# Kernel tuning notes

Measured on AMD Instinct MI355X. Metric: run time of the kernel, lower is better.

Reference implementation:

```python
import jax, jax.numpy as jnp
import numpy as np
from jax import lax

DIM = 128
TOPW = 4
SCALE = DIM ** (-0.5)


def setup_inputs() -> dict:
    key = jax.random.key(0)
    kq, ki = jax.random.split(key)
    query = jax.random.normal(kq, (4, 4096, DIM), dtype=jnp.float32)
    image = jax.random.normal(ki, (4, 8192, DIM), dtype=jnp.float32)
    return {"query": query, "image": image}


def reference(query, image):
    # diff_routing=False: inputs are detached in torch; no effect on fwd values.
    # attn: (b, Nq, mn) = scaled QK^T
    attn = jnp.einsum('bqc,bmc->bqm', query, image) * SCALE
    _, topw_index = lax.top_k(attn, TOPW)  # (b, Nq, topw)
    return topw_index
```

## Files before the change

kernel.cpp:

```cpp
#include <hip/hip_runtime.h>
#include <float.h>
#include <stdint.h>


#define NBATCH 4
#define NQ 4096
#define NM 8192
#define KD 128

typedef unsigned short ushort_t;
typedef __attribute__((ext_vector_type(8))) short bf16x8;
typedef __attribute__((ext_vector_type(16))) float f32x16;

#define BETTER64(v, i, w, j) (((v) > (w)) || ((v) == (w) && (i) < (j)))

__device__ inline float fmed3(float a, float b, float c) {
#if __has_builtin(__builtin_amdgcn_fmed3f)
  return __builtin_amdgcn_fmed3f(a, b, c);
#else
  return fmaxf(fminf(a, b), fminf(fmaxf(a, b), c));
#endif
}

__device__ inline ushort_t f2bf(float f) {
  unsigned u = __float_as_uint(f);
  u += 0x7fffu + ((u >> 16) & 1u);
  return (ushort_t)(u >> 16);
}

__global__ __launch_bounds__(256) void wr_cvt(const float* __restrict__ qry,
                                              const float* __restrict__ img,
                                              ushort_t* __restrict__ qb,
                                              int4* __restrict__ ib) {
  const int blk = (int)blockIdx.x;
  const int tid = (int)threadIdx.x;
  if (blk < 2048) {
    const int t = blk * 256 + tid;
    const float4 v = ((const float4*)qry)[t];
    ushort4 o;
    o.x = f2bf(v.x); o.y = f2bf(v.y); o.z = f2bf(v.z); o.w = f2bf(v.w);
    ((ushort4*)qb)[t] = o;
  } else {
    const int tg = blk - 2048;
    const int b = tg >> 8;
    const int tile = tg & 255;
    __shared__ __align__(16) ushort_t T[32 * 128];
    {
      const int r = tid >> 3;
      const int seg = tid & 7;
      const float* src = img + ((size_t)(b * NM + tile * 32 + r)) * KD + seg * 16;
      ushort_t tmp[16];
#pragma unroll
      for (int i = 0; i < 4; ++i) {
        const float4 v = ((const float4*)src)[i];
        tmp[i * 4 + 0] = f2bf(v.x);
        tmp[i * 4 + 1] = f2bf(v.y);
        tmp[i * 4 + 2] = f2bf(v.z);
        tmp[i * 4 + 3] = f2bf(v.w);
      }
      const int c0 = (seg * 16 + r * 8) & 127;
      const int c1 = (seg * 16 + 8 + r * 8) & 127;
      *(int4*)&T[r * 128 + c0] = *(const int4*)&tmp[0];
      *(int4*)&T[r * 128 + c1] = *(const int4*)&tmp[8];
    }
    __syncthreads();
    int4* dstt = ib + ((size_t)b * 256 + tile) * 512;
#pragma unroll
    for (int h = 0; h < 2; ++h) {
      const int n = tid + h * 256;
      const int c = n >> 6;
      const int l = n & 63;
      const int ml = l & 31;
      const int col = (c * 16 + (l >> 5) * 8 + ml * 8) & 127;
      dstt[n] = *(const int4*)&T[ml * 128 + col];
    }
  }
}

__global__ __launch_bounds__(512, 2) void wr_mfma(const float* __restrict__ qry,
                                                  const float* __restrict__ img,
                                                  const ushort_t* __restrict__ qb,
                                                  const int4* __restrict__ ib,
                                                  int* __restrict__ out) {
  const int bid = (int)blockIdx.x;
  const int b = (bid & 7) >> 1;
  const int qt = ((bid >> 3) << 1) | (bid & 1);
  const int qbase = qt * 32;

  const int tid = (int)threadIdx.x;
  const int lane = tid & 63;
  const int w = tid >> 6;
  const int qc = lane & 31;
  const int kh = lane >> 5;

  const ushort_t* Qb = qb + ((size_t)b * NQ + qbase) * KD;
  const int4* ibc = ib + (size_t)b * 131072;

  bf16x8 bfrag[8];
  {
    const ushort_t* p = Qb + (size_t)qc * KD + kh * 8;
#pragma unroll
    for (int c = 0; c < 8; ++c) bfrag[c] = *(const bf16x8*)(p + c * 16);
  }

  float tva[4], tvb[4];
#pragma unroll
  for (int s = 0; s < 4; ++s) { tva[s] = -FLT_MAX; tvb[s] = -FLT_MAX; }

  bf16x8 bufA[8], bufB[8];

  auto loadTile = [&](bf16x8* buf, int T) {
    const int4* p = ibc + ((((w * 32 + T) << 9)) + lane);
#pragma unroll
    for (int c = 0; c < 8; ++c) buf[c] = *(const bf16x8*)(p + c * 64);
  };

  auto compute = [&](const bf16x8* buf, int vb) {
    f32x16 acc;
#pragma unroll
    for (int r = 0; r < 16; ++r) acc[r] = 0.0f;
#pragma unroll
    for (int c = 0; c < 8; ++c)
      acc = __builtin_amdgcn_mfma_f32_32x32x16_bf16(buf[c], bfrag[c], acc, 0, 0, 0);
#pragma unroll
    for (int r = 0; r < 16; ++r) {
      const int rc = (r & 3) + 8 * (r >> 2);
      const unsigned kb =
          (__float_as_uint(acc[r]) & 0xFFFFF800u) | (unsigned)(vb - rc);
      const float key = __uint_as_float(kb);
      if (r & 1) {
        tvb[3] = fmed3(key, tvb[2], tvb[3]);
        tvb[2] = fmed3(key, tvb[1], tvb[2]);
        tvb[1] = fmed3(key, tvb[0], tvb[1]);
        tvb[0] = fmaxf(tvb[0], key);
      } else {
        tva[3] = fmed3(key, tva[2], tva[3]);
        tva[2] = fmed3(key, tva[1], tva[2]);
        tva[1] = fmed3(key, tva[0], tva[1]);
        tva[0] = fmaxf(tva[0], key);
      }
    }
  };

  int vb = 2047 - 4 * kh;
  loadTile(bufA, 0);
  loadTile(bufB, 1);
  for (int T = 0; T < 32; T += 2) {
    compute(bufA, vb);
    if (T + 2 < 32) loadTile(bufA, T + 2);
    compute(bufB, vb - 32);
    if (T + 3 < 32) loadTile(bufB, T + 3);
    vb -= 64;
  }

#pragma unroll
  for (int e = 0; e < 4; ++e) {
    const float key = tvb[e];
    tva[3] = fmed3(key, tva[2], tva[3]);
    tva[2] = fmed3(key, tva[1], tva[2]);
    tva[1] = fmed3(key, tva[0], tva[1]);
    tva[0] = fmaxf(tva[0], key);
  }

  {
    float keys[4];
#pragma unroll
    for (int e = 0; e < 4; ++e) keys[e] = __shfl_down(tva[e], 32, 64);
#pragma unroll
    for (int e = 0; e < 4; ++e) {
      const float key = keys[e];
      tva[3] = fmed3(key, tva[2], tva[3]);
      tva[2] = fmed3(key, tva[1], tva[2]);
      tva[1] = fmed3(key, tva[0], tva[1]);
      tva[0] = fmaxf(tva[0], key);
    }
  }

  __shared__ float ck[32][33];
  __shared__ int top8[32][8];
  __shared__ double pd[32][8];
  __shared__ int pi[32][8];

  if (kh == 0) {
#pragma unroll
    for (int s = 0; s < 4; ++s) ck[qc][w * 4 + s] = tva[s];
  }
  __syncthreads();

  for (int p = tid; p < 1024; p += 512) {
    const int q = p >> 5;
    const int j = p & 31;
    const float k = ck[q][j];
    int rank = 0;
#pragma unroll 8
    for (int i = 0; i < 32; ++i) {
      const float o = ck[q][i];
      rank += (o > k) || (o == k && i < j);
    }
    if (rank < 8) {
      const unsigned bits = __float_as_uint(k);
      top8[q][rank] = (j >> 2) * 1024 + 2047 - (int)(bits & 0x7FFu);
    }
  }
  __syncthreads();

  if (tid < 256) {
    const int q = tid >> 3;
    const int slot = tid & 7;
    const int m = top8[q][slot];
    const float* qrow = qry + ((size_t)b * NQ + qbase + q) * KD;
    const float* irow = img + ((size_t)b * NM + m) * KD;
    double s0 = 0.0, s1 = 0.0, s2 = 0.0, s3 = 0.0;
#pragma unroll
    for (int k = 0; k < KD; k += 4) {
      const float4 xv = *(const float4*)(qrow + k);
      const float4 yv = *(const float4*)(irow + k);
      s0 = fma((double)xv.x, (double)yv.x, s0);
      s1 = fma((double)xv.y, (double)yv.y, s1);
      s2 = fma((double)xv.z, (double)yv.z, s2);
      s3 = fma((double)xv.w, (double)yv.w, s3);
    }
    pd[q][slot] = (s0 + s1) + (s2 + s3);
    pi[q][slot] = m;
  }
  __syncthreads();

  if (tid < 32) {
    const int q = tid;
    double fv[4];
    int fi[4];
#pragma unroll
    for (int e = 0; e < 4; ++e) { fv[e] = -DBL_MAX; fi[e] = 0x7fffffff; }
    for (int sl = 0; sl < 8; ++sl) {
      const double v = pd[q][sl];
      const int m = pi[q][sl];
      const bool b0 = BETTER64(v, m, fv[0], fi[0]);
      const bool b1 = BETTER64(v, m, fv[1], fi[1]);
      const bool b2 = BETTER64(v, m, fv[2], fi[2]);
      const bool b3 = BETTER64(v, m, fv[3], fi[3]);
      fv[3] = b2 ? fv[2] : (b3 ? v : fv[3]);
      fi[3] = b2 ? fi[2] : (b3 ? m : fi[3]);
      fv[2] = b1 ? fv[1] : (b2 ? v : fv[2]);
      fi[2] = b1 ? fi[1] : (b2 ? m : fi[2]);
      fv[1] = b0 ? fv[0] : (b1 ? v : fv[1]);
      fi[1] = b0 ? fi[0] : (b1 ? m : fi[1]);
      fv[0] = b0 ? v : fv[0];
      fi[0] = b0 ? m : fi[0];
    }
    int4 o;
    o.x = fi[0]; o.y = fi[1]; o.z = fi[2]; o.w = fi[3];
    *(int4*)(out + ((size_t)b * NQ + qbase + q) * 4) = o;
  }
}

#define QT 64
#define MT 128
#define KC 64
#define NTHREADS 512

__global__ __launch_bounds__(NTHREADS) void wr_main(const float* __restrict__ qry,
                                                    const float* __restrict__ img,
                                                    int* __restrict__ out) {
  __shared__ __align__(16) float A_lds[KD * QT];
  __shared__ __align__(16) float B_lds[KC * MT];

  const int t = (int)threadIdx.x;
  const int b = (int)blockIdx.x >> 6;
  const int qbase = ((int)blockIdx.x & 63) * QT;

  const float* qp = qry + ((size_t)b * NQ + qbase) * KD;
  const float* ip = img + (size_t)b * NM * KD;

  {
    const int r = t >> 3;
    const int kc = t & 7;
    const float* src = qp + (size_t)r * KD;
#pragma unroll
    for (int i = 0; i < 4; ++i) {
      const int k0 = kc * 4 + i * 32;
      const float4 v = *(const float4*)(src + k0);
      A_lds[(k0 + 0) * QT + r] = v.x;
      A_lds[(k0 + 1) * QT + r] = v.y;
      A_lds[(k0 + 2) * QT + r] = v.z;
      A_lds[(k0 + 3) * QT + r] = v.w;
    }
  }

  const int qi = t >> 5;
  const int mi = t & 31;

  float tv[4][4];
  int ti[4][4];
#pragma unroll
  for (int j = 0; j < 4; ++j)
#pragma unroll
    for (int s = 0; s < 4; ++s) { tv[j][s] = -FLT_MAX; ti[j][s] = 0x7fffffff; }

  for (int tile = 0; tile < NM / MT; ++tile) {
    const int mbase = tile * MT;
    float acc[4][4];
#pragma unroll
    for (int j = 0; j < 4; ++j)
#pragma unroll
      for (int s = 0; s < 4; ++s) acc[j][s] = 0.0f;

    for (int kb = 0; kb < KD; kb += KC) {
      __syncthreads();
      {
        const int r = t >> 2;
        const int kc = t & 3;
        const float* src = ip + (size_t)(mbase + r) * KD + kb;
#pragma unroll
        for (int i = 0; i < 4; ++i) {
          const int k0 = kc * 4 + i * 16;
          const float4 v = *(const float4*)(src + k0);
          B_lds[(k0 + 0) * MT + r] = v.x;
          B_lds[(k0 + 1) * MT + r] = v.y;
          B_lds[(k0 + 2) * MT + r] = v.z;
          B_lds[(k0 + 3) * MT + r] = v.w;
        }
      }
      __syncthreads();

#pragma unroll 8
      for (int k = 0; k < KC; ++k) {
        const float4 av = *(const float4*)&A_lds[(kb + k) * QT + qi * 4];
        const float4 bv = *(const float4*)&B_lds[k * MT + mi * 4];
        acc[0][0] = fmaf(av.x, bv.x, acc[0][0]);
        acc[0][1] = fmaf(av.x, bv.y, acc[0][1]);
        acc[0][2] = fmaf(av.x, bv.z, acc[0][2]);
        acc[0][3] = fmaf(av.x, bv.w, acc[0][3]);
        acc[1][0] = fmaf(av.y, bv.x, acc[1][0]);
        acc[1][1] = fmaf(av.y, bv.y, acc[1][1]);
        acc[1][2] = fmaf(av.y, bv.z, acc[1][2]);
        acc[1][3] = fmaf(av.y, bv.w, acc[1][3]);
        acc[2][0] = fmaf(av.z, bv.x, acc[2][0]);
        acc[2][1] = fmaf(av.z, bv.y, acc[2][1]);
        acc[2][2] = fmaf(av.z, bv.z, acc[2][2]);
        acc[2][3] = fmaf(av.z, bv.w, acc[2][3]);
        acc[3][0] = fmaf(av.w, bv.x, acc[3][0]);
        acc[3][1] = fmaf(av.w, bv.y, acc[3][1]);
        acc[3][2] = fmaf(av.w, bv.z, acc[3][2]);
        acc[3][3] = fmaf(av.w, bv.w, acc[3][3]);
      }
    }

#pragma unroll
    for (int j = 0; j < 4; ++j) {
#pragma unroll
      for (int s = 0; s < 4; ++s) {
        const float v = acc[j][s];
        const int m = mbase + mi * 4 + s;
        const bool b0 = v > tv[j][0];
        const bool b1 = v > tv[j][1];
        const bool b2 = v > tv[j][2];
        const bool b3 = v > tv[j][3];
        tv[j][3] = b2 ? tv[j][2] : (b3 ? v : tv[j][3]);
        ti[j][3] = b2 ? ti[j][2] : (b3 ? m : ti[j][3]);
        tv[j][2] = b1 ? tv[j][1] : (b2 ? v : tv[j][2]);
        ti[j][2] = b1 ? ti[j][1] : (b2 ? m : ti[j][2]);
        tv[j][1] = b0 ? tv[j][0] : (b1 ? v : tv[j][1]);
        ti[j][1] = b0 ? ti[j][0] : (b1 ? m : ti[j][1]);
        tv[j][0] = b0 ? v : tv[j][0];
        ti[j][0] = b0 ? m : ti[j][0];
      }
    }
  }

  __syncthreads();
  int* idx_lds = (int*)B_lds;
#pragma unroll
  for (int j = 0; j < 4; ++j)
#pragma unroll
    for (int s = 0; s < 4; ++s)
      idx_lds[(qi * 4 + j) * 128 + mi * 4 + s] = ti[j][s];
  __syncthreads();

  double* pv = (double*)A_lds;
  int* piL = (int*)(A_lds + 4096);
  {
    const int r = t >> 3;
    const int slot = t & 7;
    const float* qrow = qp + (size_t)r * KD;
    double bv[4];
    int bi[4];
#pragma unroll
    for (int e = 0; e < 4; ++e) { bv[e] = -DBL_MAX; bi[e] = 0x7fffffff; }

    for (int c = 0; c < 16; ++c) {
      const int m = idx_lds[r * 128 + slot * 16 + c];
      const float* irow = ip + (size_t)m * KD;
      double s0 = 0.0, s1 = 0.0, s2 = 0.0, s3 = 0.0;
#pragma unroll
      for (int k = 0; k < KD; k += 4) {
        const float4 xv = *(const float4*)(qrow + k);
        const float4 yv = *(const float4*)(irow + k);
        s0 = fma((double)xv.x, (double)yv.x, s0);
        s1 = fma((double)xv.y, (double)yv.y, s1);
        s2 = fma((double)xv.z, (double)yv.z, s2);
        s3 = fma((double)xv.w, (double)yv.w, s3);
      }
      const double v = (s0 + s1) + (s2 + s3);
      const bool b0 = BETTER64(v, m, bv[0], bi[0]);
      const bool b1 = BETTER64(v, m, bv[1], bi[1]);
      const bool b2 = BETTER64(v, m, bv[2], bi[2]);
      const bool b3 = BETTER64(v, m, bv[3], bi[3]);
      bv[3] = b2 ? bv[2] : (b3 ? v : bv[3]);
      bi[3] = b2 ? bi[2] : (b3 ? m : bi[3]);
      bv[2] = b1 ? bv[1] : (b2 ? v : bv[2]);
      bi[2] = b1 ? bi[1] : (b2 ? m : bi[2]);
      bv[1] = b0 ? bv[0] : (b1 ? v : bv[1]);
      bi[1] = b0 ? bi[0] : (b1 ? m : bi[1]);
      bv[0] = b0 ? v : bv[0];
      bi[0] = b0 ? m : bi[0];
    }
#pragma unroll
    for (int e = 0; e < 4; ++e) {
      pv[t * 4 + e] = bv[e];
      piL[t * 4 + e] = bi[e];
    }
  }
  __syncthreads();

  if (t < QT) {
    double fv[4];
    int fi[4];
#pragma unroll
    for (int e = 0; e < 4; ++e) { fv[e] = -DBL_MAX; fi[e] = 0x7fffffff; }
    for (int sl = 0; sl < 8; ++sl) {
#pragma unroll
      for (int e = 0; e < 4; ++e) {
        const double v = pv[(t * 8 + sl) * 4 + e];
        const int m = piL[(t * 8 + sl) * 4 + e];
        const bool b0 = BETTER64(v, m, fv[0], fi[0]);
        const bool b1 = BETTER64(v, m, fv[1], fi[1]);
        const bool b2 = BETTER64(v, m, fv[2], fi[2]);
        const bool b3 = BETTER64(v, m, fv[3], fi[3]);
        fv[3] = b2 ? fv[2] : (b3 ? v : fv[3]);
        fi[3] = b2 ? fi[2] : (b3 ? m : fi[3]);
        fv[2] = b1 ? fv[1] : (b2 ? v : fv[2]);
        fi[2] = b1 ? fi[1] : (b2 ? m : fi[2]);
        fv[1] = b0 ? fv[0] : (b1 ? v : fv[1]);
        fi[1] = b0 ? fi[0] : (b1 ? m : fi[1]);
        fv[0] = b0 ? v : fv[0];
        fi[0] = b0 ? m : fi[0];
      }
    }
    int4 o;
    o.x = fi[0]; o.y = fi[1]; o.z = fi[2]; o.w = fi[3];
    *(int4*)(out + ((size_t)b * NQ + qbase + t) * 4) = o;
  }
}

extern "C" void kernel_launch(void* const* d_in, const int* in_sizes, int n_in,
                              void* d_out, int out_size, void* d_ws, size_t ws_size,
                              hipStream_t stream) {
  const float* qry = (const float*)d_in[0];
  const float* img = (const float*)d_in[1];
  int* out = (int*)d_out;

  const size_t qbBytes = (size_t)NBATCH * NQ * KD * sizeof(ushort_t);
  const size_t ibBytes = (size_t)NBATCH * NM * KD * sizeof(ushort_t);

  if (ws_size >= qbBytes + ibBytes) {
    ushort_t* qb = (ushort_t*)d_ws;
    int4* ib = (int4*)((char*)d_ws + qbBytes);
    wr_cvt<<<3072, 256, 0, stream>>>(qry, img, qb, ib);
    wr_mfma<<<512, 512, 0, stream>>>(qry, img, qb, ib, out);
  } else {
    wr_main<<<NBATCH * (NQ / QT), NTHREADS, 0, stream>>>(qry, img, out);
  }
}
```

Measured before the change: 144.7 us.

## Switch to 16x16x32 MFMA with triple-buffered image loads

Replaces the 32x32x16 bf16 MFMA over 32-key tiles with 16x16x32 MFMAs processing 16 image rows against two 16-query fragments. The image repack layout changes to match the new operand shape, and loads become triple-buffered in smaller 16-row chunks. The intent is to cut accumulator register pressure and shorten the dependency chain between the MFMA and the top-4 selection, improving latency hiding. In exchange there are more loop steps and an extra shuffle-merge stage in the final per-query reduction.

```diff
diff --git a/kernel.cpp b/kernel.cpp
--- a/kernel.cpp
+++ b/kernel.cpp
@@ -10,7 +10,7 @@
 
 typedef unsigned short ushort_t;
 typedef __attribute__((ext_vector_type(8))) short bf16x8;
-typedef __attribute__((ext_vector_type(16))) float f32x16;
+typedef __attribute__((ext_vector_type(4))) float f32x4;
 
 #define BETTER64(v, i, w, j) (((v) > (w)) || ((v) == (w) && (i) < (j)))
 
@@ -68,11 +68,12 @@
 #pragma unroll
     for (int h = 0; h < 2; ++h) {
       const int n = tid + h * 256;
-      const int c = n >> 6;
       const int l = n & 63;
-      const int ml = l & 31;
-      const int col = (c * 16 + (l >> 5) * 8 + ml * 8) & 127;
-      dstt[n] = *(const int4*)&T[ml * 128 + col];
+      const int ks = (n >> 6) & 3;
+      const int htl = n >> 8;
+      const int row = htl * 16 + (l & 15);
+      const int col = ks * 32 + (l >> 4) * 8;
+      dstt[n] = *(const int4*)&T[row * 128 + ((col + row * 8) & 127)];
     }
   }
 }
@@ -90,89 +91,109 @@
   const int tid = (int)threadIdx.x;
   const int lane = tid & 63;
   const int w = tid >> 6;
-  const int qc = lane & 31;
-  const int kh = lane >> 5;
+  const int q15 = lane & 15;
+  const int quad = lane >> 4;
 
   const ushort_t* Qb = qb + ((size_t)b * NQ + qbase) * KD;
   const int4* ibc = ib + (size_t)b * 131072;
 
-  bf16x8 bfrag[8];
+  bf16x8 bfrag0[4], bfrag1[4];
+#pragma unroll
+  for (int ks = 0; ks < 4; ++ks) {
+    bfrag0[ks] = *(const bf16x8*)(Qb + (size_t)q15 * KD + ks * 32 + quad * 8);
+    bfrag1[ks] = *(const bf16x8*)(Qb + (size_t)(16 + q15) * KD + ks * 32 + quad * 8);
+  }
+
+  float tq0[4], tq1[4];
+#pragma unroll
+  for (int s = 0; s < 4; ++s) { tq0[s] = -FLT_MAX; tq1[s] = -FLT_MAX; }
+
+  bf16x8 B0[4], B1[4], B2[4];
+
+  auto loadH = [&](bf16x8* R, int h) {
+    const int4* p = ibc + (((w * 64 + h) << 8) + lane);
+#pragma unroll
+    for (int ks = 0; ks < 4; ++ks) R[ks] = *(const bf16x8*)(p + ks * 64);
+  };
+
+  int hl = 3;
+  int vb = 2047 - 4 * quad;
+
+  auto step = [&](bf16x8* R) {
+    f32x4 a0 = {0.f, 0.f, 0.f, 0.f}, a1 = {0.f, 0.f, 0.f, 0.f};
+#pragma unroll
+    for (int ks = 0; ks < 4; ++ks) {
+      a0 = __builtin_amdgcn_mfma_f32_16x16x32_bf16(R[ks], bfrag0[ks], a0, 0, 0, 0);
+      a1 = __builtin_amdgcn_mfma_f32_16x16x32_bf16(R[ks], bfrag1[ks], a1, 0, 0, 0);
+    }
+    if (hl < 64) loadH(R, hl);
+    ++hl;
+#pragma unroll
+    for (int r = 0; r < 4; ++r) {
+      const unsigned kr = (unsigned)(vb - r);
+      const float ka =
+          __uint_as_float((__float_as_uint(a0[r]) & 0xFFFFF800u) | kr);
+      tq0[3] = fmed3(ka, tq0[2], tq0[3]);
+      tq0[2] = fmed3(ka, tq0[1], tq0[2]);
+      tq0[1] = fmed3(ka, tq0[0], tq0[1]);
+      tq0[0] = fmaxf(tq0[0], ka);
+      const float kb =
+          __uint_as_float((__float_as_uint(a1[r]) & 0xFFFFF800u) | kr);
+      tq1[3] = fmed3(kb, tq1[2], tq1[3]);
+      tq1[2] = fmed3(kb, tq1[1], tq1[2]);
+      tq1[1] = fmed3(kb, tq1[0], tq1[1]);
+      tq1[0] = fmaxf(tq1[0], kb);
+    }
+    vb -= 16;
+  };
+
+  loadH(B0, 0);
+  loadH(B1, 1);
+  loadH(B2, 2);
+  for (int g = 0; g < 21; ++g) { step(B0); step(B1); step(B2); }
+  step(B0);
+
   {
-    const ushort_t* p = Qb + (size_t)qc * KD + kh * 8;
-#pragma unroll
-    for (int c = 0; c < 8; ++c) bfrag[c] = *(const bf16x8*)(p + c * 16);
-  }
-
-  float tva[4], tvb[4];
-#pragma unroll
-  for (int s = 0; s < 4; ++s) { tva[s] = -FLT_MAX; tvb[s] = -FLT_MAX; }
-
-  bf16x8 bufA[8], bufB[8];
-
-  auto loadTile = [&](bf16x8* buf, int T) {
-    const int4* p = ibc + ((((w * 32 + T) << 9)) + lane);
-#pragma unroll
-    for (int c = 0; c < 8; ++c) buf[c] = *(const bf16x8*)(p + c * 64);
-  };
-
-  auto compute = [&](const bf16x8* buf, int vb) {
-    f32x16 acc;
-#pragma unroll
-    for (int r = 0; r < 16; ++r) acc[r] = 0.0f;
-#pragma unroll
-    for (int c = 0; c < 8; ++c)
-      acc = __builtin_amdgcn_mfma_f32_32x32x16_bf16(buf[c], bfrag[c], acc, 0, 0, 0);
-#pragma unroll
-    for (int r = 0; r < 16; ++r) {
-      const int rc = (r & 3) + 8 * (r >> 2);
-      const unsigned kb =
-          (__float_as_uint(acc[r]) & 0xFFFFF800u) | (unsigned)(vb - rc);
-      const float key = __uint_as_float(kb);
-      if (r & 1) {
-        tvb[3] = fmed3(key, tvb[2], tvb[3]);
-        tvb[2] = fmed3(key, tvb[1], tvb[2]);
-        tvb[1] = fmed3(key, tvb[0], tvb[1]);
-        tvb[0] = fmaxf(tvb[0], key);
-      } else {
-        tva[3] = fmed3(key, tva[2], tva[3]);
-        tva[2] = fmed3(key, tva[1], tva[2]);
-        tva[1] = fmed3(key, tva[0], tva[1]);
-        tva[0] = fmaxf(tva[0], key);
-      }
-    }
-  };
-
-  int vb = 2047 - 4 * kh;
-  loadTile(bufA, 0);
-  loadTile(bufB, 1);
-  for (int T = 0; T < 32; T += 2) {
-    compute(bufA, vb);
-    if (T + 2 < 32) loadTile(bufA, T + 2);
-    compute(bufB, vb - 32);
-    if (T + 3 < 32) loadTile(bufB, T + 3);
-    vb -= 64;
-  }
-
-#pragma unroll
-  for (int e = 0; e < 4; ++e) {
-    const float key = tvb[e];
-    tva[3] = fmed3(key, tva[2], tva[3]);
-    tva[2] = fmed3(key, tva[1], tva[2]);
-    tva[1] = fmed3(key, tva[0], tva[1]);
-    tva[0] = fmaxf(tva[0], key);
-  }
-
-  {
-    float keys[4];
-#pragma unroll
-    for (int e = 0; e < 4; ++e) keys[e] = __shfl_down(tva[e], 32, 64);
+    float k4[4];
+#pragma unroll
+    for (int e = 0; e < 4; ++e) k4[e] = __shfl_down(tq0[e], 32, 64);
 #pragma unroll
     for (int e = 0; e < 4; ++e) {
-      const float key = keys[e];
-      tva[3] = fmed3(key, tva[2], tva[3]);
-      tva[2] = fmed3(key, tva[1], tva[2]);
-      tva[1] = fmed3(key, tva[0], tva[1]);
-      tva[0] = fmaxf(tva[0], key);
+      const float k = k4[e];
+      tq0[3] = fmed3(k, tq0[2], tq0[3]);
+      tq0[2] = fmed3(k, tq0[1], tq0[2]);
+      tq0[1] = fmed3(k, tq0[0], tq0[1]);
+      tq0[0] = fmaxf(tq0[0], k);
+    }
+#pragma unroll
+    for (int e = 0; e < 4; ++e) k4[e] = __shfl_down(tq0[e], 16, 64);
+#pragma unroll
+    for (int e = 0; e < 4; ++e) {
+      const float k = k4[e];
+      tq0[3] = fmed3(k, tq0[2], tq0[3]);
+      tq0[2] = fmed3(k, tq0[1], tq0[2]);
+      tq0[1] = fmed3(k, tq0[0], tq0[1]);
+      tq0[0] = fmaxf(tq0[0], k);
+    }
+#pragma unroll
+    for (int e = 0; e < 4; ++e) k4[e] = __shfl_down(tq1[e], 32, 64);
+#pragma unroll
+    for (int e = 0; e < 4; ++e) {
+      const float k = k4[e];
+      tq1[3] = fmed3(k, tq1[2], tq1[3]);
+      tq1[2] = fmed3(k, tq1[1], tq1[2]);
+      tq1[1] = fmed3(k, tq1[0], tq1[1]);
+      tq1[0] = fmaxf(tq1[0], k);
+    }
+#pragma unroll
+    for (int e = 0; e < 4; ++e) k4[e] = __shfl_down(tq1[e], 16, 64);
+#pragma unroll
+    for (int e = 0; e < 4; ++e) {
+      const float k = k4[e];
+      tq1[3] = fmed3(k, tq1[2], tq1[3]);
+      tq1[2] = fmed3(k, tq1[1], tq1[2]);
+      tq1[1] = fmed3(k, tq1[0], tq1[1]);
+      tq1[0] = fmaxf(tq1[0], k);
     }
   }
 
@@ -181,9 +202,12 @@
   __shared__ double pd[32][8];
   __shared__ int pi[32][8];
 
-  if (kh == 0) {
-#pragma unroll
-    for (int s = 0; s < 4; ++s) ck[qc][w * 4 + s] = tva[s];
+  if (lane < 16) {
+#pragma unroll
+    for (int s = 0; s < 4; ++s) {
+      ck[q15][w * 4 + s] = tq0[s];
+      ck[16 + q15][w * 4 + s] = tq1[s];
+    }
   }
   __syncthreads();
 
```

New measurement: 138.9 us. 1.04x faster.
